# Kernel tuning notes

Measured on AMD Instinct MI355X. Metric: run time of the kernel, lower is better.

Reference implementation:

```python
import jax, jax.numpy as jnp
import numpy as np

B, N_, K_, Q_, H = 32, 20, 10, 2048, 1024
EPS = 1e-5  # torch LayerNorm default


def setup_inputs() -> dict:
    key = jax.random.key(0)
    k1, k2 = jax.random.split(key)
    return {
        "support": jax.random.normal(k1, (B * N_ * K_, H), dtype=jnp.float32),
        "query": jax.random.normal(k2, (B * Q_, H), dtype=jnp.float32),
        "gamma": jnp.ones((H,), dtype=jnp.float32),
        "beta": jnp.zeros((H,), dtype=jnp.float32),
        "N": N_,
        "K": K_,
        "Q_total": Q_,
    }


def _layernorm(x, gamma, beta):
    m = jnp.mean(x, axis=-1, keepdims=True)
    v = jnp.mean(jnp.square(x - m), axis=-1, keepdims=True)  # biased variance
    return (x - m) * jax.lax.rsqrt(v + EPS) * gamma + beta


def reference(support, query, gamma, beta, N, K, Q_total):
    H_ = gamma.shape[0]
    s = _layernorm(support, gamma, beta).reshape(-1, N * K, H_)   # (B, NK, H)
    q = _layernorm(query, gamma, beta).reshape(-1, Q_total, H_)   # (B, Q, H)
    # broadcast dot-product similarity, fused as a batched matmul
    z = jnp.einsum("bqh,bkh->bqk", q, s)                          # (B, Q, NK)
    z = z.reshape(-1, Q_total, N, K)
    logits = jnp.max(z, axis=-1)                                  # max over K -> (B, Q, N)
    minn = jnp.min(logits, axis=-1)                               # min over N -> (B, Q)
    logits = jnp.concatenate([logits, minn[:, :, None] - 1.0], axis=2)  # (B, Q, N+1)
    pred = jnp.argmax(logits.reshape(-1, N + 1), axis=1)
    return logits, pred
```

## Files before the change

kernel.cpp:

```cpp
#include <hip/hip_runtime.h>
#include <hip/hip_bf16.h>

#define Hd   1024
#define Bd   32
#define Nd   20
#define Kd   10
#define NKd  200
#define NKP  208
#define Qd   2048
#define BM   64
#define ZLD  209
#define EPSf 1e-5f
#define TAU  0.02f
#define MAXF 2048
#define TCH  (832 * 8)

typedef __attribute__((ext_vector_type(8))) short bf16x8;
typedef __attribute__((ext_vector_type(4))) float f32x4;

#define SWZ(row, k8) (((row) * 32) + (((k8) ^ ((row) & 3)) * 8))

static __device__ __forceinline__ unsigned short f2bf(float f) {
  union { float f; unsigned u; } c; c.f = f;
  unsigned r = c.u + 0x7FFFu + ((c.u >> 16) & 1u);
  return (unsigned short)(r >> 16);
}
static __device__ __forceinline__ float bf2f(unsigned short h) {
  union { unsigned u; float f; } c; c.u = ((unsigned)h) << 16;
  return c.f;
}
static __device__ __forceinline__ void gload_lds16(const void* g, void* l) {
  __builtin_amdgcn_global_load_lds(
      (const __attribute__((address_space(1))) unsigned int*)g,
      (__attribute__((address_space(3))) unsigned int*)l, 16, 0, 0);
}

__global__ __launch_bounds__(256) void ln_support(const float* __restrict__ x,
                                                  const float* __restrict__ gamma,
                                                  const float* __restrict__ beta,
                                                  unsigned short* __restrict__ y_hi,
                                                  unsigned short* __restrict__ y_lo,
                                                  float* __restrict__ Gv,
                                                  float* __restrict__ Bv) {
  int wave = threadIdx.x >> 6, lane = threadIdx.x & 63;
  int p = blockIdx.x * 4 + wave;
  int b = p / NKP, rr = p - b * NKP;
  int T0 = lane >> 1;
  int k8base = (lane & 1) * 2;
  int sw = rr & 3;
  size_t chunkbase = (size_t)b * 32 * TCH + (size_t)T0 * TCH + (size_t)rr * 32;

  if (rr >= NKd) {
    bf16x8 z8 = {0, 0, 0, 0, 0, 0, 0, 0};
#pragma unroll
    for (int pr = 0; pr < 2; ++pr) {
      size_t off = chunkbase + (size_t)(((k8base + pr) ^ sw) * 8);
      *(bf16x8*)(y_hi + off) = z8;
      *(bf16x8*)(y_lo + off) = z8;
    }
    if (lane == 0) { Gv[p] = 0.f; Bv[p] = 0.f; }
    return;
  }
  const float4* xr = (const float4*)(x + ((size_t)b * NKd + rr) * Hd);
  const float4* gr = (const float4*)gamma;
  const float4* br = (const float4*)beta;
  float4 v[4];
  float s = 0.f, ss = 0.f;
#pragma unroll
  for (int j = 0; j < 4; ++j) {
    v[j] = xr[lane * 4 + j];
    s  += v[j].x + v[j].y + v[j].z + v[j].w;
    ss += v[j].x * v[j].x + v[j].y * v[j].y + v[j].z * v[j].z + v[j].w * v[j].w;
  }
#pragma unroll
  for (int o = 32; o; o >>= 1) { s += __shfl_xor(s, o, 64); ss += __shfl_xor(ss, o, 64); }
  float mean = s * (1.0f / Hd);
  float rstd = rsqrtf(ss * (1.0f / Hd) - mean * mean + EPSf);

  float nx[16];
  float sg = 0.f, sb = 0.f;
#pragma unroll
  for (int j = 0; j < 4; ++j) {
    float4 g = gr[lane * 4 + j], bb = br[lane * 4 + j];
    float xv[4] = {v[j].x, v[j].y, v[j].z, v[j].w};
    float gv4[4] = {g.x, g.y, g.z, g.w};
    float bv4[4] = {bb.x, bb.y, bb.z, bb.w};
#pragma unroll
    for (int e = 0; e < 4; ++e) {
      float n = (xv[e] - mean) * rstd * gv4[e] + bv4[e];
      nx[j * 4 + e] = n;
      sg += n * gv4[e];
      sb += n * bv4[e];
    }
  }
#pragma unroll
  for (int pr = 0; pr < 2; ++pr) {
    bf16x8 ph, pl;
#pragma unroll
    for (int e = 0; e < 8; ++e) {
      float n = nx[pr * 8 + e];
      unsigned short h = f2bf(n);
      ph[e] = (short)h;
      pl[e] = (short)f2bf(n - bf2f(h));
    }
    size_t off = chunkbase + (size_t)(((k8base + pr) ^ sw) * 8);
    *(bf16x8*)(y_hi + off) = ph;
    *(bf16x8*)(y_lo + off) = pl;
  }
#pragma unroll
  for (int o = 32; o; o >>= 1) { sg += __shfl_xor(sg, o, 64); sb += __shfl_xor(sb, o, 64); }
  if (lane == 0) { Gv[p] = sg; Bv[p] = sb; }
}

__global__ __launch_bounds__(256, 3) void gemm_reduce(
    const float* __restrict__ query,
    const unsigned short* __restrict__ s_hi, const unsigned short* __restrict__ s_lo,
    const float* __restrict__ gamma,
    const float* __restrict__ Gv, const float* __restrict__ Bv,
    float* __restrict__ out_logits, float* __restrict__ out_pred,
    int* __restrict__ flag_cnt, int* __restrict__ flag_list) {
  __shared__ union {
    unsigned short B[2][2][TCH];
    float z[BM][ZLD];
  } sm;
  __shared__ float qstat[4][16][2];

  int lin = blockIdx.x;
  int xcd = lin & 7, sl = lin >> 3;
  int b = xcd + 8 * (sl >> 5);
  int m0 = (sl & 31) * BM;
  int t = threadIdx.x;
  int wave = t >> 6, lane = t & 63;
  int m = lane & 15, quad = lane >> 4;

  const size_t qrow0 = (size_t)b * Qd + m0;
  const float* qptr = query + (qrow0 + wave * 16 + m) * Hd;
  const unsigned short* hb = s_hi + (size_t)b * 32 * TCH;
  const unsigned short* lb = s_lo + (size_t)b * 32 * TCH;

  f32x4 acc[13];
#pragma unroll
  for (int i = 0; i < 13; ++i) acc[i] = (f32x4){0.f, 0.f, 0.f, 0.f};
  float sx = 0.f, sxx = 0.f;

  for (int j = wave; j < 26; j += 4) {
    int pl = j >= 13 ? 1 : 0, jj = j - pl * 13;
    const unsigned short* src = (pl ? lb : hb) + (size_t)jj * 512 + lane * 8;
    gload_lds16(src, &sm.B[0][pl][jj * 512]);
  }

  for (int T = 0; T < 32; ++T) {
    int u = T & 1;
    int ko = T * 32 + quad * 8;
    const float4* qp = (const float4*)(qptr + ko);
    float4 x0 = qp[0], x1 = qp[1];
    const float4* gp = (const float4*)(gamma + ko);
    float4 g0 = gp[0], g1 = gp[1];
    float xs[8] = {x0.x, x0.y, x0.z, x0.w, x1.x, x1.y, x1.z, x1.w};
    float gs[8] = {g0.x, g0.y, g0.z, g0.w, g1.x, g1.y, g1.z, g1.w};
    bf16x8 ah, al;
#pragma unroll
    for (int j = 0; j < 8; ++j) {
      sx += xs[j];
      sxx = fmaf(xs[j], xs[j], sxx);
      float uu = xs[j] * gs[j];
      unsigned short h = f2bf(uu);
      ah[j] = (short)h;
      al[j] = (short)f2bf(uu - bf2f(h));
    }

    __syncthreads();

    if (T + 1 < 32) {
      size_t toff = (size_t)(T + 1) * TCH;
      for (int j = wave; j < 26; j += 4) {
        int pl = j >= 13 ? 1 : 0, jj = j - pl * 13;
        const unsigned short* src = (pl ? lb : hb) + toff + (size_t)jj * 512 + lane * 8;
        gload_lds16(src, &sm.B[1 - u][pl][jj * 512]);
      }
    }

    const unsigned short* Bh = sm.B[u][0];
    const unsigned short* Bl = sm.B[u][1];
#pragma unroll
    for (int nt = 0; nt < 13; ++nt) {
      int rw = nt * 16 + m;
      bf16x8 bh = *(const bf16x8*)&Bh[SWZ(rw, quad)];
      bf16x8 bl = *(const bf16x8*)&Bl[SWZ(rw, quad)];
      acc[nt] = __builtin_amdgcn_mfma_f32_16x16x32_bf16(ah, bh, acc[nt], 0, 0, 0);
      acc[nt] = __builtin_amdgcn_mfma_f32_16x16x32_bf16(al, bh, acc[nt], 0, 0, 0);
      acc[nt] = __builtin_amdgcn_mfma_f32_16x16x32_bf16(ah, bl, acc[nt], 0, 0, 0);
    }
  }

  sx  += __shfl_xor(sx, 16, 64);  sxx += __shfl_xor(sxx, 16, 64);
  sx  += __shfl_xor(sx, 32, 64);  sxx += __shfl_xor(sxx, 32, 64);
  float mean = sx * (1.0f / Hd);
  float rstd = rsqrtf(sxx * (1.0f / Hd) - mean * mean + EPSf);
  if (quad == 0) { qstat[wave][m][0] = mean; qstat[wave][m][1] = rstd; }
  __syncthreads();

  float Gc[13], Bc[13];
#pragma unroll
  for (int nt = 0; nt < 13; ++nt) {
    int col = b * NKP + nt * 16 + m;
    Gc[nt] = Gv[col];
    Bc[nt] = Bv[col];
  }
#pragma unroll
  for (int r = 0; r < 4; ++r) {
    int row = quad * 4 + r;
    float mn = qstat[wave][row][0], rs = qstat[wave][row][1];
    float mrs = mn * rs;
#pragma unroll
    for (int nt = 0; nt < 13; ++nt)
      sm.z[wave * 16 + row][nt * 16 + m] = rs * acc[nt][r] - mrs * Gc[nt] + Bc[nt];
  }
  __syncthreads();

  for (int i = t; i < BM * Nd; i += 256) {
    int row = i / Nd, g = i - row * Nd;
    float* zp = &sm.z[row][g * Kd];
    float mx = zp[0];
#pragma unroll
    for (int j = 1; j < Kd; ++j) mx = fmaxf(mx, zp[j]);
    zp[0] = mx;
  }
  __syncthreads();

  if (t < BM) {
    int row = t;
    float mn = 3.4e38f, v1 = -3.4e38f, v2 = -3.4e38f;
    int best = 0;
    size_t orow = qrow0 + row;
    float* lp = out_logits + orow * (Nd + 1);
#pragma unroll
    for (int n = 0; n < Nd; ++n) {
      float v = sm.z[row][n * Kd];
      lp[n] = v;
      mn = fminf(mn, v);
      if (v > v1) { v2 = v1; v1 = v; best = n; }
      else v2 = fmaxf(v2, v);
    }
    lp[Nd] = mn - 1.0f;
    out_pred[orow] = (float)best;
    if (v1 - v2 < TAU) {
      int idx = atomicAdd(flag_cnt, 1);
      if (idx < MAXF) flag_list[idx] = (int)orow;
    }
  }
}

__global__ __launch_bounds__(256) void refine_pred(
    const float* __restrict__ query, const float* __restrict__ support,
    const float* __restrict__ gamma, const float* __restrict__ beta,
    const int* __restrict__ flag_cnt, const int* __restrict__ flag_list,
    float* __restrict__ out_pred) {
  __shared__ double A[Hd];
  __shared__ double red[16];
  __shared__ double zbuf[NKd];
  __shared__ double gmax[Nd];
  int cnt = *flag_cnt; if (cnt > MAXF) cnt = MAXF;
  if ((int)blockIdx.x >= cnt) return;
  int qrow = flag_list[blockIdx.x];
  int b = qrow / Qd;
  int t = threadIdx.x, lane = t & 63, w = t >> 6;
  const float* qx = query + (size_t)qrow * Hd;
  float xv[4];
  double sx = 0.0, sxx = 0.0;
#pragma unroll
  for (int i = 0; i < 4; ++i) {
    xv[i] = qx[t * 4 + i];
    sx += (double)xv[i]; sxx += (double)xv[i] * (double)xv[i];
  }
#pragma unroll
  for (int o = 32; o; o >>= 1) { sx += __shfl_xor(sx, o, 64); sxx += __shfl_xor(sxx, o, 64); }
  if (lane == 0) { red[w] = sx; red[8 + w] = sxx; }
  __syncthreads();
  double m = (red[0] + red[1] + red[2] + red[3]) * (1.0 / Hd);
  double var = (red[8] + red[9] + red[10] + red[11]) * (1.0 / Hd) - m * m;
  double r = 1.0 / sqrt(var + 1e-5);
  double s1 = 0.0, s2 = 0.0;
#pragma unroll
  for (int i = 0; i < 4; ++i) {
    int j = t * 4 + i;
    double g = (double)gamma[j], be = (double)beta[j];
    double qn = ((double)xv[i] - m) * r * g + be;
    double a = qn * g;
    A[j] = a; s1 += a; s2 += qn * be;
  }
#pragma unroll
  for (int o = 32; o; o >>= 1) { s1 += __shfl_xor(s1, o, 64); s2 += __shfl_xor(s2, o, 64); }
  __syncthreads();
  if (lane == 0) { red[w] = s1; red[8 + w] = s2; }
  __syncthreads();
  double S1 = red[0] + red[1] + red[2] + red[3];
  double S2 = red[8] + red[9] + red[10] + red[11];
  const float* sbase = support + (size_t)b * NKd * Hd;
  for (int row = w; row < NKd; row += 4) {
    const float* xr = sbase + (size_t)row * Hd;
    double tx = 0.0, txx = 0.0, tax = 0.0;
#pragma unroll
    for (int i = 0; i < 16; ++i) {
      int j = lane + i * 64;
      double x = (double)xr[j];
      tx += x; txx += x * x; tax += A[j] * x;
    }
#pragma unroll
    for (int o = 32; o; o >>= 1) {
      tx += __shfl_xor(tx, o, 64); txx += __shfl_xor(txx, o, 64); tax += __shfl_xor(tax, o, 64);
    }
    if (lane == 0) {
      double mm = tx * (1.0 / Hd);
      double vv = txx * (1.0 / Hd) - mm * mm;
      double rr = 1.0 / sqrt(vv + 1e-5);
      zbuf[row] = rr * (tax - mm * S1) + S2;
    }
  }
  __syncthreads();
  if (t < Nd) {
    double mx = zbuf[t * Kd];
#pragma unroll
    for (int j = 1; j < Kd; ++j) mx = fmax(mx, zbuf[t * Kd + j]);
    gmax[t] = mx;
  }
  __syncthreads();
  if (t == 0) {
    double bv = gmax[0]; int best = 0;
#pragma unroll
    for (int n = 1; n < Nd; ++n) if (gmax[n] > bv) { bv = gmax[n]; best = n; }
    out_pred[qrow] = (float)best;
  }
}

extern "C" void kernel_launch(void* const* d_in, const int* in_sizes, int n_in,
                              void* d_out, int out_size, void* d_ws, size_t ws_size,
                              hipStream_t stream) {
  const float* support = (const float*)d_in[0];
  const float* query   = (const float*)d_in[1];
  const float* gamma   = (const float*)d_in[2];
  const float* beta    = (const float*)d_in[3];

  float* out = (float*)d_out;
  float* out_logits = out;
  float* out_pred   = out + (size_t)Bd * Qd * (Nd + 1);

  const size_t plane = (size_t)Bd * 32 * TCH;
  unsigned short* s_hi = (unsigned short*)d_ws;
  unsigned short* s_lo = s_hi + plane;
  char* p = (char*)(s_lo + plane);
  float* Gv = (float*)p;            p += (size_t)Bd * NKP * sizeof(float);
  float* Bv = (float*)p;            p += (size_t)Bd * NKP * sizeof(float);
  int* flag_cnt = (int*)p;
  int* flag_list = (int*)(p + 256);

  hipMemsetAsync(flag_cnt, 0, sizeof(int), stream);
  ln_support<<<(Bd * NKP) / 4, 256, 0, stream>>>(support, gamma, beta, s_hi, s_lo, Gv, Bv);
  gemm_reduce<<<Qd / BM * Bd, 256, 0, stream>>>(query, s_hi, s_lo, gamma, Gv, Bv,
                                                out_logits, out_pred, flag_cnt, flag_list);
  refine_pred<<<MAXF, 256, 0, stream>>>(query, support, gamma, beta, flag_cnt, flag_list, out_pred);
}
```

Measured before the change: 553.6 us.

## Double query tile per block to reuse support B fragments across two row groups

Raises the query tile from 64 to 128 rows per block, so each wave computes two 16-row MFMA tiles that share every B fragment read from LDS. This halves the number of blocks and the support-chunk DMA traffic per query row. It also prefetches the next query slice into registers before the MFMA loop, switches the hi/lo bf16 split to packed v_cvt_pk_bf16_f32, changes the LDS swizzle, and writes the epilogue in two passes through the 64-row z buffer. In exchange the accumulator count doubles and the launch bound drops to 2 blocks per CU, so register pressure and occupancy may limit overlap.

```diff
diff --git a/kernel.cpp b/kernel.cpp
--- a/kernel.cpp
+++ b/kernel.cpp
@@ -8,17 +8,21 @@
 #define NKd  200
 #define NKP  208
 #define Qd   2048
-#define BM   64
+#define BM   128
+#define ZR   64
 #define ZLD  209
 #define EPSf 1e-5f
 #define TAU  0.02f
 #define MAXF 2048
 #define TCH  (832 * 8)
+#define PLB  (TCH * 2)
+#define BUFB (2 * PLB)
 
 typedef __attribute__((ext_vector_type(8))) short bf16x8;
 typedef __attribute__((ext_vector_type(4))) float f32x4;
-
-#define SWZ(row, k8) (((row) * 32) + (((k8) ^ ((row) & 3)) * 8))
+typedef __attribute__((ext_vector_type(4))) unsigned int u32x4;
+
+#define SWS(r) (((r) ^ ((r) >> 2)) & 3)
 
 static __device__ __forceinline__ unsigned short f2bf(float f) {
   union { float f; unsigned u; } c; c.f = f;
@@ -28,6 +32,14 @@
 static __device__ __forceinline__ float bf2f(unsigned short h) {
   union { unsigned u; float f; } c; c.u = ((unsigned)h) << 16;
   return c.f;
+}
+static __device__ __forceinline__ float ubitf(unsigned u) {
+  union { unsigned u; float f; } c; c.u = u; return c.f;
+}
+static __device__ __forceinline__ unsigned cvtpk_bf16(float a, float b) {
+  unsigned r;
+  asm("v_cvt_pk_bf16_f32 %0, %1, %2" : "=v"(r) : "v"(a), "v"(b));
+  return r;
 }
 static __device__ __forceinline__ void gload_lds16(const void* g, void* l) {
   __builtin_amdgcn_global_load_lds(
@@ -47,7 +59,7 @@
   int b = p / NKP, rr = p - b * NKP;
   int T0 = lane >> 1;
   int k8base = (lane & 1) * 2;
-  int sw = rr & 3;
+  int sw = SWS(rr);
   size_t chunkbase = (size_t)b * 32 * TCH + (size_t)T0 * TCH + (size_t)rr * 32;
 
   if (rr >= NKd) {
@@ -112,93 +124,128 @@
   if (lane == 0) { Gv[p] = sg; Bv[p] = sb; }
 }
 
-__global__ __launch_bounds__(256, 3) void gemm_reduce(
+static __device__ __forceinline__ void split8(float4 xa, float4 xb, float4 ga, float4 gb,
+                                              float& sx, float& sxx,
+                                              bf16x8& AH, bf16x8& AL) {
+  float x[8] = {xa.x, xa.y, xa.z, xa.w, xb.x, xb.y, xb.z, xb.w};
+  float g[8] = {ga.x, ga.y, ga.z, ga.w, gb.x, gb.y, gb.z, gb.w};
+  float u[8];
+#pragma unroll
+  for (int e = 0; e < 8; ++e) {
+    sx += x[e];
+    sxx = fmaf(x[e], x[e], sxx);
+    u[e] = x[e] * g[e];
+  }
+  unsigned h[4], l[4];
+#pragma unroll
+  for (int p = 0; p < 4; ++p) {
+    h[p] = cvtpk_bf16(u[2 * p], u[2 * p + 1]);
+    float r0 = ubitf(h[p] << 16);
+    float r1 = ubitf(h[p] & 0xFFFF0000u);
+    l[p] = cvtpk_bf16(u[2 * p] - r0, u[2 * p + 1] - r1);
+  }
+  AH = __builtin_bit_cast(bf16x8, (u32x4){h[0], h[1], h[2], h[3]});
+  AL = __builtin_bit_cast(bf16x8, (u32x4){l[0], l[1], l[2], l[3]});
+}
+
+__global__ __launch_bounds__(256, 2) void gemm_reduce(
     const float* __restrict__ query,
     const unsigned short* __restrict__ s_hi, const unsigned short* __restrict__ s_lo,
     const float* __restrict__ gamma,
     const float* __restrict__ Gv, const float* __restrict__ Bv,
     float* __restrict__ out_logits, float* __restrict__ out_pred,
     int* __restrict__ flag_cnt, int* __restrict__ flag_list) {
-  __shared__ union {
+  __shared__ __align__(16) union {
     unsigned short B[2][2][TCH];
-    float z[BM][ZLD];
+    float z[ZR][ZLD];
   } sm;
-  __shared__ float qstat[4][16][2];
 
   int lin = blockIdx.x;
   int xcd = lin & 7, sl = lin >> 3;
-  int b = xcd + 8 * (sl >> 5);
-  int m0 = (sl & 31) * BM;
+  int b = xcd + 8 * (sl >> 4);
+  int m0 = (sl & 15) * BM;
   int t = threadIdx.x;
   int wave = t >> 6, lane = t & 63;
   int m = lane & 15, quad = lane >> 4;
 
   const size_t qrow0 = (size_t)b * Qd + m0;
-  const float* qptr = query + (qrow0 + wave * 16 + m) * Hd;
+  const float* qf0 = query + (qrow0 + wave * 32 + m) * Hd;
+  const float* qf1 = qf0 + 16 * Hd;
   const unsigned short* hb = s_hi + (size_t)b * 32 * TCH;
   const unsigned short* lb = s_lo + (size_t)b * 32 * TCH;
 
-  f32x4 acc[13];
-#pragma unroll
-  for (int i = 0; i < 13; ++i) acc[i] = (f32x4){0.f, 0.f, 0.f, 0.f};
-  float sx = 0.f, sxx = 0.f;
-
-  for (int j = wave; j < 26; j += 4) {
-    int pl = j >= 13 ? 1 : 0, jj = j - pl * 13;
-    const unsigned short* src = (pl ? lb : hb) + (size_t)jj * 512 + lane * 8;
-    gload_lds16(src, &sm.B[0][pl][jj * 512]);
-  }
+  char* ldsB = (char*)&sm.B[0][0][0];
+  const char* rdB = ldsB + m * 64 + ((quad ^ SWS(m)) * 16);
+
+  auto issue_dma = [&](int Tn, int bufsel) {
+    size_t toff = (size_t)Tn * TCH;
+    char* dstb = ldsB + bufsel * BUFB;
+#pragma unroll
+    for (int i = 0; i < 7; ++i) {
+      int j = wave + i * 4;
+      if (j < 26) {
+        int pl = j >= 13 ? 1 : 0, jj = j - pl * 13;
+        const unsigned short* src = (pl ? lb : hb) + toff + (size_t)jj * 512 + lane * 8;
+        gload_lds16(src, dstb + pl * PLB + jj * 1024);
+      }
+    }
+  };
+
+  float4 xq00, xq01, xq10, xq11, gq0, gq1;
+  auto loadA = [&](int T) {
+    int ko = T * 32 + quad * 8;
+    const float4* g4 = (const float4*)(gamma + ko);
+    gq0 = g4[0]; gq1 = g4[1];
+    const float4* q0 = (const float4*)(qf0 + ko);
+    xq00 = q0[0]; xq01 = q0[1];
+    const float4* q1 = (const float4*)(qf1 + ko);
+    xq10 = q1[0]; xq11 = q1[1];
+  };
+
+  f32x4 acc0[13], acc1[13];
+#pragma unroll
+  for (int i = 0; i < 13; ++i) {
+    acc0[i] = (f32x4){0.f, 0.f, 0.f, 0.f};
+    acc1[i] = (f32x4){0.f, 0.f, 0.f, 0.f};
+  }
+  float sx0 = 0.f, sxx0 = 0.f, sx1 = 0.f, sxx1 = 0.f;
+
+  issue_dma(0, 0);
+  loadA(0);
 
   for (int T = 0; T < 32; ++T) {
     int u = T & 1;
-    int ko = T * 32 + quad * 8;
-    const float4* qp = (const float4*)(qptr + ko);
-    float4 x0 = qp[0], x1 = qp[1];
-    const float4* gp = (const float4*)(gamma + ko);
-    float4 g0 = gp[0], g1 = gp[1];
-    float xs[8] = {x0.x, x0.y, x0.z, x0.w, x1.x, x1.y, x1.z, x1.w};
-    float gs[8] = {g0.x, g0.y, g0.z, g0.w, g1.x, g1.y, g1.z, g1.w};
-    bf16x8 ah, al;
-#pragma unroll
-    for (int j = 0; j < 8; ++j) {
-      sx += xs[j];
-      sxx = fmaf(xs[j], xs[j], sxx);
-      float uu = xs[j] * gs[j];
-      unsigned short h = f2bf(uu);
-      ah[j] = (short)h;
-      al[j] = (short)f2bf(uu - bf2f(h));
-    }
-
     __syncthreads();
 
-    if (T + 1 < 32) {
-      size_t toff = (size_t)(T + 1) * TCH;
-      for (int j = wave; j < 26; j += 4) {
-        int pl = j >= 13 ? 1 : 0, jj = j - pl * 13;
-        const unsigned short* src = (pl ? lb : hb) + toff + (size_t)jj * 512 + lane * 8;
-        gload_lds16(src, &sm.B[1 - u][pl][jj * 512]);
-      }
-    }
-
-    const unsigned short* Bh = sm.B[u][0];
-    const unsigned short* Bl = sm.B[u][1];
+    if (T + 1 < 32) issue_dma(T + 1, 1 - u);
+
+    bf16x8 ah0, al0, ah1, al1;
+    split8(xq00, xq01, gq0, gq1, sx0, sxx0, ah0, al0);
+    split8(xq10, xq11, gq0, gq1, sx1, sxx1, ah1, al1);
+    if (T + 1 < 32) loadA(T + 1);
+
+    const char* Bu = rdB + (u ? BUFB : 0);
 #pragma unroll
     for (int nt = 0; nt < 13; ++nt) {
-      int rw = nt * 16 + m;
-      bf16x8 bh = *(const bf16x8*)&Bh[SWZ(rw, quad)];
-      bf16x8 bl = *(const bf16x8*)&Bl[SWZ(rw, quad)];
-      acc[nt] = __builtin_amdgcn_mfma_f32_16x16x32_bf16(ah, bh, acc[nt], 0, 0, 0);
-      acc[nt] = __builtin_amdgcn_mfma_f32_16x16x32_bf16(al, bh, acc[nt], 0, 0, 0);
-      acc[nt] = __builtin_amdgcn_mfma_f32_16x16x32_bf16(ah, bl, acc[nt], 0, 0, 0);
-    }
-  }
-
-  sx  += __shfl_xor(sx, 16, 64);  sxx += __shfl_xor(sxx, 16, 64);
-  sx  += __shfl_xor(sx, 32, 64);  sxx += __shfl_xor(sxx, 32, 64);
-  float mean = sx * (1.0f / Hd);
-  float rstd = rsqrtf(sxx * (1.0f / Hd) - mean * mean + EPSf);
-  if (quad == 0) { qstat[wave][m][0] = mean; qstat[wave][m][1] = rstd; }
-  __syncthreads();
+      bf16x8 bh = *(const bf16x8*)(Bu + nt * 1024);
+      bf16x8 bl = *(const bf16x8*)(Bu + PLB + nt * 1024);
+      acc0[nt] = __builtin_amdgcn_mfma_f32_16x16x32_bf16(ah0, bh, acc0[nt], 0, 0, 0);
+      acc1[nt] = __builtin_amdgcn_mfma_f32_16x16x32_bf16(ah1, bh, acc1[nt], 0, 0, 0);
+      acc0[nt] = __builtin_amdgcn_mfma_f32_16x16x32_bf16(al0, bh, acc0[nt], 0, 0, 0);
+      acc1[nt] = __builtin_amdgcn_mfma_f32_16x16x32_bf16(al1, bh, acc1[nt], 0, 0, 0);
+      acc0[nt] = __builtin_amdgcn_mfma_f32_16x16x32_bf16(ah0, bl, acc0[nt], 0, 0, 0);
+      acc1[nt] = __builtin_amdgcn_mfma_f32_16x16x32_bf16(ah1, bl, acc1[nt], 0, 0, 0);
+    }
+  }
+
+  sx0 += __shfl_xor(sx0, 16, 64);  sxx0 += __shfl_xor(sxx0, 16, 64);
+  sx0 += __shfl_xor(sx0, 32, 64);  sxx0 += __shfl_xor(sxx0, 32, 64);
+  sx1 += __shfl_xor(sx1, 16, 64);  sxx1 += __shfl_xor(sxx1, 16, 64);
+  sx1 += __shfl_xor(sx1, 32, 64);  sxx1 += __shfl_xor(sxx1, 32, 64);
+  float mean0 = sx0 * (1.0f / Hd);
+  float rstd0 = rsqrtf(sxx0 * (1.0f / Hd) - mean0 * mean0 + EPSf);
+  float mean1 = sx1 * (1.0f / Hd);
+  float rstd1 = rsqrtf(sxx1 * (1.0f / Hd) - mean1 * mean1 + EPSf);
 
   float Gc[13], Bc[13];
 #pragma unroll
@@ -207,46 +254,63 @@
     Gc[nt] = Gv[col];
     Bc[nt] = Bv[col];
   }
-#pragma unroll
-  for (int r = 0; r < 4; ++r) {
-    int row = quad * 4 + r;
-    float mn = qstat[wave][row][0], rs = qstat[wave][row][1];
-    float mrs = mn * rs;
-#pragma unroll
-    for (int nt = 0; nt < 13; ++nt)
-      sm.z[wave * 16 + row][nt * 16 + m] = rs * acc[nt][r] - mrs * Gc[nt] + Bc[nt];
-  }
-  __syncthreads();
-
-  for (int i = t; i < BM * Nd; i += 256) {
-    int row = i / Nd, g = i - row * Nd;
-    float* zp = &sm.z[row][g * Kd];
-    float mx = zp[0];
-#pragma unroll
-    for (int j = 1; j < Kd; ++j) mx = fmaxf(mx, zp[j]);
-    zp[0] = mx;
-  }
-  __syncthreads();
-
-  if (t < BM) {
-    int row = t;
-    float mn = 3.4e38f, v1 = -3.4e38f, v2 = -3.4e38f;
-    int best = 0;
-    size_t orow = qrow0 + row;
-    float* lp = out_logits + orow * (Nd + 1);
-#pragma unroll
-    for (int n = 0; n < Nd; ++n) {
-      float v = sm.z[row][n * Kd];
-      lp[n] = v;
-      mn = fminf(mn, v);
-      if (v > v1) { v2 = v1; v1 = v; best = n; }
-      else v2 = fmaxf(v2, v);
-    }
-    lp[Nd] = mn - 1.0f;
-    out_pred[orow] = (float)best;
-    if (v1 - v2 < TAU) {
-      int idx = atomicAdd(flag_cnt, 1);
-      if (idx < MAXF) flag_list[idx] = (int)orow;
+
+#pragma unroll
+  for (int pass = 0; pass < 2; ++pass) {
+    __syncthreads();
+    if ((wave >> 1) == pass) {
+      int zb = (wave & 1) * 32;
+#pragma unroll
+      for (int r = 0; r < 4; ++r) {
+        int lr = quad * 4 + r;
+        {
+          float mn = __shfl(mean0, lr, 16), rs = __shfl(rstd0, lr, 16);
+          float mrs = mn * rs;
+#pragma unroll
+          for (int nt = 0; nt < 13; ++nt)
+            sm.z[zb + lr][nt * 16 + m] = rs * acc0[nt][r] - mrs * Gc[nt] + Bc[nt];
+        }
+        {
+          float mn = __shfl(mean1, lr, 16), rs = __shfl(rstd1, lr, 16);
+          float mrs = mn * rs;
+#pragma unroll
+          for (int nt = 0; nt < 13; ++nt)
+            sm.z[zb + 16 + lr][nt * 16 + m] = rs * acc1[nt][r] - mrs * Gc[nt] + Bc[nt];
+        }
+      }
+    }
+    __syncthreads();
+
+    for (int i = t; i < ZR * Nd; i += 256) {
+      int row = i / Nd, g = i - row * Nd;
+      float* zp = &sm.z[row][g * Kd];
+      float mx = zp[0];
+#pragma unroll
+      for (int j = 1; j < Kd; ++j) mx = fmaxf(mx, zp[j]);
+      zp[0] = mx;
+    }
+    __syncthreads();
+
+    if (t < ZR) {
+      int row = t;
+      float mn = 3.4e38f, v1 = -3.4e38f, v2 = -3.4e38f;
+      int best = 0;
+      size_t orow = qrow0 + pass * ZR + row;
+      float* lp = out_logits + orow * (Nd + 1);
+#pragma unroll
+      for (int n = 0; n < Nd; ++n) {
+        float v = sm.z[row][n * Kd];
+        lp[n] = v;
+        mn = fminf(mn, v);
+        if (v > v1) { v2 = v1; v1 = v; best = n; }
+        else v2 = fmaxf(v2, v);
+      }
+      lp[Nd] = mn - 1.0f;
+      out_pred[orow] = (float)best;
+      if (v1 - v2 < TAU) {
+        int idx = atomicAdd(flag_cnt, 1);
+        if (idx < MAXF) flag_list[idx] = (int)orow;
+      }
     }
   }
 }
```

New measurement: 488.3 us. -11.8%, faster.
